# Optimization experiments

Hardware: AMD Instinct MI355X
Metric: run time of the kernel (lower is better)

Reference implementation:

```python
import jax, jax.numpy as jnp
import numpy as np

M, N = 4096, 4096

def _make_expk(n):
    k = np.arange(n, dtype=np.float64) * np.pi / (2.0 * n)
    return jnp.asarray(np.stack([np.cos(k), np.sin(k)], axis=-1), dtype=jnp.float32)

def setup_inputs() -> dict:
    key = jax.random.key(0)
    x = jax.random.normal(key, (M, N), dtype=jnp.float32)
    return {"x": x, "expkM": _make_expk(M), "expkN": _make_expk(N)}

def _idct_last(X, expk):
    """1D IDCT (inverse of unnormalized DCT-II) along last axis via Makhoul's
    N-point FFT trick. expk[k] = (cos, sin) of pi*k/(2N), i.e. e^{j pi k/(2N)}."""
    n = X.shape[-1]
    Xv = X * 0.5
    # V[k] = (Xv[k] - j*Xv[n-k]) * e^{j pi k/(2n)}, with imag part 0 at k=0
    tail = -jnp.flip(Xv, axis=-1)[..., :-1]
    Vi = jnp.concatenate([jnp.zeros_like(Xv[..., :1]), tail], axis=-1)
    W = expk[:, 0] + 1j * expk[:, 1]
    V = (Xv + 1j * Vi) * W
    v = jnp.fft.ifft(V, axis=-1).real.astype(X.dtype)
    # de-interleave: out[2m] = v[m], out[2m+1] = v[n-1-m]
    out = jnp.zeros_like(X)
    out = out.at[..., 0::2].set(v[..., : n - n // 2])
    out = out.at[..., 1::2].set(jnp.flip(v, axis=-1)[..., : n // 2])
    return out

def reference(x, expkM, expkN):
    # separable 2D IDCT: last axis (N) then first axis (M)
    y = _idct_last(x, expkN)
    y = _idct_last(y.T, expkM).T
    return y
```

## Files before the change

### kernel.cpp

```cpp
#include <hip/hip_runtime.h>
#include <math.h>


#define TT 256

constexpr float W64R[32] = {
    1.0f, 0.995184726672197f, 0.980785280403230f, 0.956940335732209f,
    0.923879532511287f, 0.881921264348355f, 0.831469612302545f, 0.773010453362737f,
    0.707106781186548f, 0.634393284163645f, 0.555570233019602f, 0.471396736825998f,
    0.382683432365090f, 0.290284677254462f, 0.195090322016128f, 0.0980171403295606f,
    0.0f, -0.0980171403295606f, -0.195090322016128f, -0.290284677254462f,
    -0.382683432365090f, -0.471396736825998f, -0.555570233019602f, -0.634393284163645f,
    -0.707106781186548f, -0.773010453362737f, -0.831469612302545f, -0.881921264348355f,
    -0.923879532511287f, -0.956940335732209f, -0.980785280403230f, -0.995184726672197f};
constexpr float W64I[32] = {
    0.0f, 0.0980171403295606f, 0.195090322016128f, 0.290284677254462f,
    0.382683432365090f, 0.471396736825998f, 0.555570233019602f, 0.634393284163645f,
    0.707106781186548f, 0.773010453362737f, 0.831469612302545f, 0.881921264348355f,
    0.923879532511287f, 0.956940335732209f, 0.980785280403230f, 0.995184726672197f,
    1.0f, 0.995184726672197f, 0.980785280403230f, 0.956940335732209f,
    0.923879532511287f, 0.881921264348355f, 0.831469612302545f, 0.773010453362737f,
    0.707106781186548f, 0.634393284163645f, 0.555570233019602f, 0.471396736825998f,
    0.382683432365090f, 0.290284677254462f, 0.195090322016128f, 0.0980171403295606f};

__device__ __forceinline__ constexpr int brev(int x, int bits) {
    int r = 0;
    for (int i = 0; i < bits; ++i) { r = (r << 1) | (x & 1); x >>= 1; }
    return r;
}

__device__ __forceinline__ float vadd(float a, float b) { return a + b; }
__device__ __forceinline__ float vsub(float a, float b) { return a - b; }
__device__ __forceinline__ float vmul(float a, float s) { return a * s; }
__device__ __forceinline__ float2 vadd(float2 a, float2 b) { return make_float2(a.x + b.x, a.y + b.y); }
__device__ __forceinline__ float2 vsub(float2 a, float2 b) { return make_float2(a.x - b.x, a.y - b.y); }
__device__ __forceinline__ float2 vmul(float2 a, float s) { return make_float2(a.x * s, a.y * s); }

template <int NP, typename V>
__device__ __forceinline__ void fft_dif(V* re, V* im) {
#pragma unroll
    for (int h = NP / 2; h >= 1; h >>= 1) {
#pragma unroll
        for (int b = 0; b < NP; b += 2 * h) {
#pragma unroll
            for (int k = 0; k < h; ++k) {
                V ur = re[b + k], ui = im[b + k];
                V vr = re[b + k + h], vi = im[b + k + h];
                V dr = vsub(ur, vr), di = vsub(ui, vi);
                re[b + k] = vadd(ur, vr);
                im[b + k] = vadd(ui, vi);
                float wr = W64R[k * (32 / h)], wi = W64I[k * (32 / h)];
                re[b + k + h] = vsub(vmul(dr, wr), vmul(di, wi));
                im[b + k + h] = vadd(vmul(dr, wi), vmul(di, wr));
            }
        }
    }
}

__global__ void tw_init_kernel(float2* __restrict__ tw2048,
                               float2* __restrict__ ca, float2* __restrict__ cb,
                               float2* __restrict__ cc, float2* __restrict__ cd) {
    int k = blockIdx.x * TT + threadIdx.x;
    const double s = 0.5 / 4096.0;
    double aw = M_PI * (double)k / 2048.0;
    double wr = cos(aw), wi = sin(aw);
    double a1 = M_PI * (double)k / 8192.0;
    double e1r = cos(a1), e1i = sin(a1);
    double a2 = M_PI * (double)(k + 2048) / 8192.0;
    double e2r = cos(a2), e2i = sin(a2);
    double Ar = s * ((1.0 - wi) * e1r - wr * e1i);
    double Ai = s * ((1.0 - wi) * e1i + wr * e1r);
    double Br = (k == 0) ? 0.0 : Ai;
    double Bi = (k == 0) ? 0.0 : -Ar;
    double Cr = s * ((1.0 + wi) * e2r + wr * e2i);
    double Ci = s * ((1.0 + wi) * e2i - wr * e2r);
    ca[k] = make_float2((float)Ar, (float)Ai);
    cb[k] = make_float2((float)Br, (float)Bi);
    cc[k] = make_float2((float)Cr, (float)Ci);
    cd[k] = make_float2((float)Ci, (float)-Cr);
    double at = M_PI * (double)k / 1024.0;
    tw2048[k] = make_float2((float)cos(at), (float)sin(at));
}

__global__ __launch_bounds__(TT, 4) void col_a_kernel(
    const float* __restrict__ x,
    const float2* __restrict__ ca, const float2* __restrict__ cb,
    const float2* __restrict__ cc, const float2* __restrict__ cd,
    const float2* __restrict__ tw2048, float2* __restrict__ T1) {
    int c = blockIdx.x * 64 + threadIdx.x;
    int k1 = blockIdx.y * 4 + threadIdx.y;
    float fr[32], fi[32];
#pragma unroll
    for (int k2 = 0; k2 < 32; ++k2) {
        int k = k1 + 64 * k2;
        float xa = x[(size_t)k * 4096 + c];
        float xb = x[(size_t)((4096 - k) & 4095) * 4096 + c];
        float xc = x[(size_t)(2048 + k) * 4096 + c];
        float xd = x[(size_t)(2048 - k) * 4096 + c];
        float2 A = ca[k], B = cb[k], C = cc[k], D = cd[k];
        fr[k2] = A.x * xa + B.x * xb + C.x * xc + D.x * xd;
        fi[k2] = A.y * xa + B.y * xb + C.y * xc + D.y * xd;
    }
    fft_dif<32, float>(fr, fi);
#pragma unroll
    for (int j = 0; j < 32; ++j) {
        int n2 = brev(j, 5);
        float2 w = tw2048[k1 * n2];
        float2 o = make_float2(fr[j] * w.x - fi[j] * w.y,
                               fr[j] * w.y + fi[j] * w.x);
        T1[(size_t)(k1 * 32 + n2) * 4096 + c] = o;
    }
}

__global__ __launch_bounds__(TT, 4) void col_b_kernel(
    const float2* __restrict__ T1, float* __restrict__ out) {
    __shared__ float2 EO[2][32][64];
    int tx = threadIdx.x;
    int ty = threadIdx.y;
    int tz = ty & 1;
    int g  = ty >> 1;
    int c = blockIdx.x * 64 + tx;
    int n2 = blockIdx.y * 2 + g;
    float fr[32], fi[32];
#pragma unroll
    for (int a = 0; a < 32; ++a) {
        int k1 = 2 * a + tz;
        float2 v = T1[(size_t)(k1 * 32 + n2) * 4096 + c];
        fr[a] = v.x; fi[a] = v.y;
    }
    fft_dif<32, float>(fr, fi);
#pragma unroll
    for (int gg = 0; gg < 2; ++gg) {
        if (g == gg) {
#pragma unroll
            for (int j = 0; j < 32; ++j) {
                int n = brev(j, 5);
                float vr = fr[j], vi = fi[j];
                if (tz) {
                    float wr = W64R[n], wi = W64I[n];
                    float t2 = vr * wr - vi * wi;
                    vi = vr * wi + vi * wr;
                    vr = t2;
                }
                EO[tz][n][tx] = make_float2(vr, vi);
            }
        }
        __syncthreads();
        if (g == gg) {
#pragma unroll
            for (int n = 0; n < 32; ++n) {
                float2 E  = EO[0][n][tx];
                float2 WO = EO[1][n][tx];
                float zr, zi;
                if (tz == 0) { zr = E.x + WO.x; zi = E.y + WO.y; }
                else         { zr = E.x - WO.x; zi = E.y - WO.y; }
                int n1 = tz * 32 + n;
                int m = 32 * n1 + n2;
                int r_re = (n1 < 32) ? 4 * m     : 8191 - 4 * m;
                int r_im = (n1 < 32) ? 4 * m + 2 : 8189 - 4 * m;
                out[(size_t)r_re * 4096 + c] = zr;
                out[(size_t)r_im * 4096 + c] = zi;
            }
        }
        __syncthreads();
    }
}

#define C_SQ2 0.70710678118654752440f
__device__ __forceinline__ void radix8(const float* ar, const float* ai,
                                       float* tr, float* ti) {
    float s04r = ar[0] + ar[4], s04i = ai[0] + ai[4];
    float d04r = ar[0] - ar[4], d04i = ai[0] - ai[4];
    float s26r = ar[2] + ar[6], s26i = ai[2] + ai[6];
    float d26r = ar[2] - ar[6], d26i = ai[2] - ai[6];
    float E0r = s04r + s26r, E0i = s04i + s26i;
    float E1r = d04r - d26i, E1i = d04i + d26r;
    float E2r = s04r - s26r, E2i = s04i - s26i;
    float E3r = d04r + d26i, E3i = d04i - d26r;
    float s15r = ar[1] + ar[5], s15i = ai[1] + ai[5];
    float d15r = ar[1] - ar[5], d15i = ai[1] - ai[5];
    float s37r = ar[3] + ar[7], s37i = ai[3] + ai[7];
    float d37r = ar[3] - ar[7], d37i = ai[3] - ai[7];
    float O0r = s15r + s37r, O0i = s15i + s37i;
    float O1r = d15r - d37i, O1i = d15i + d37r;
    float O2r = s15r - s37r, O2i = s15i - s37i;
    float O3r = d15r + d37i, O3i = d15i - d37r;
    float W1r = C_SQ2 * (O1r - O1i), W1i = C_SQ2 * (O1r + O1i);
    float W2r = -O2i, W2i = O2r;
    float W3r = -C_SQ2 * (O3r + O3i), W3i = C_SQ2 * (O3r - O3i);
    tr[0] = E0r + O0r; ti[0] = E0i + O0i;
    tr[4] = E0r - O0r; ti[4] = E0i - O0i;
    tr[1] = E1r + W1r; ti[1] = E1i + W1i;
    tr[5] = E1r - W1r; ti[5] = E1i - W1i;
    tr[2] = E2r + W2r; ti[2] = E2i + W2i;
    tr[6] = E2r - W2r; ti[6] = E2i - W2i;
    tr[3] = E3r + W3r; ti[3] = E3i + W3i;
    tr[7] = E3r - W3r; ti[7] = E3i - W3i;
}

__global__ __launch_bounds__(TT) void idct_rows_kernel(
    const float2* __restrict__ ca, const float2* __restrict__ cb,
    const float2* __restrict__ cc, const float2* __restrict__ cd,
    const float2* __restrict__ tw2048, float* __restrict__ io) {
    __shared__ float pool[8576];
    float* b0r = pool;
    float* b0i = pool + 2112;
    float* b1r = pool + 4224;
    float* b1i = pool + 6400;
    float* stg = pool + 4224;
    const int t = threadIdx.x;
    float* __restrict__ xr = io + (size_t)blockIdx.x * 4096;

#pragma unroll
    for (int u = 0; u < 4; ++u) {
        int idx = t + 256 * u;
        float4 v = ((const float4*)xr)[idx];
        *(float4*)&stg[4 * idx] = v;
    }
    __syncthreads();

    float zr[8], zi[8], tr[8], ti[8];
#pragma unroll
    for (int p = 0; p < 8; ++p) {
        int k = t + 256 * p;
        float xa = stg[k];
        float xb = stg[(4096 - k) & 4095];
        float xc = stg[2048 + k];
        float xd = stg[2048 - k];
        float2 A = ca[k], B = cb[k], C = cc[k], D = cd[k];
        zr[p] = A.x * xa + B.x * xb + C.x * xc + D.x * xd;
        zi[p] = A.y * xa + B.y * xb + C.y * xc + D.y * xd;
    }
    radix8(zr, zi, tr, ti);
    {
        int baseA = 8 * t + (t >> 2);
        b0r[baseA] = tr[0]; b0i[baseA] = ti[0];
#pragma unroll
        for (int q = 1; q < 8; ++q) {
            float2 w = tw2048[(t * q) & 2047];
            b0r[baseA + q] = w.x * tr[q] - w.y * ti[q];
            b0i[baseA + q] = w.x * ti[q] + w.y * tr[q];
        }
    }
    __syncthreads();
    {
        float ar[8], ai[8];
        int rb = t + (t >> 5);
#pragma unroll
        for (int p = 0; p < 8; ++p) { ar[p] = b0r[rb + 264 * p]; ai[p] = b0i[rb + 264 * p]; }
        radix8(ar, ai, tr, ti);
        int j = t >> 3, k = t & 7, wj = 8 * j;
        int baseB = 68 * j + k;
        b1r[baseB] = tr[0]; b1i[baseB] = ti[0];
#pragma unroll
        for (int q = 1; q < 8; ++q) {
            int off = baseB + 8 * q + (q >> 1);
            float2 w = tw2048[(wj * q) & 2047];
            b1r[off] = w.x * tr[q] - w.y * ti[q];
            b1i[off] = w.x * ti[q] + w.y * tr[q];
        }
    }
    __syncthreads();
    {
        float ar[8], ai[8];
        int rb = t + (t >> 4);
#pragma unroll
        for (int p = 0; p < 8; ++p) { ar[p] = b1r[rb + 272 * p]; ai[p] = b1i[rb + 272 * p]; }
        radix8(ar, ai, tr, ti);
        int j = t >> 6, wj = 64 * j, k = t & 63;
        int baseC = 528 * j + k + (k >> 5);
        b0r[baseC] = tr[0]; b0i[baseC] = ti[0];
#pragma unroll
        for (int q = 1; q < 8; ++q) {
            int off = baseC + 66 * q;
            float2 w = tw2048[(wj * q) & 2047];
            b0r[off] = w.x * tr[q] - w.y * ti[q];
            b0i[off] = w.x * ti[q] + w.y * tr[q];
        }
    }
    __syncthreads();
#pragma unroll
    for (int u = 0; u < 2; ++u) {
        int b = t + 256 * u;
        int rb = b + (b >> 5);
        int wb = b + (b >> 4);
        float a0r = b0r[rb], a0i = b0i[rb];
        float a1r = b0r[rb + 528], a1i = b0i[rb + 528];
        float a2r = b0r[rb + 1056], a2i = b0i[rb + 1056];
        float a3r = b0r[rb + 1584], a3i = b0i[rb + 1584];
        float s02r = a0r + a2r, s02i = a0i + a2i;
        float d02r = a0r - a2r, d02i = a0i - a2i;
        float s13r = a1r + a3r, s13i = a1i + a3i;
        float d13r = a1r - a3r, d13i = a1i - a3i;
        b1r[wb] = s02r + s13r;          b1i[wb] = s02i + s13i;
        b1r[wb + 544] = d02r - d13i;    b1i[wb + 544] = d02i + d13r;
        b1r[wb + 1088] = s02r - s13r;   b1i[wb + 1088] = s02i - s13i;
        b1r[wb + 1632] = d02r + d13i;   b1i[wb + 1632] = d02i - d13r;
    }
    __syncthreads();
#pragma unroll
    for (int i = 0; i < 4; ++i) {
        int s = t + 256 * i;
        int l2 = 2047 - s;
        int ms = s + (s >> 4);
        int ml = l2 + (l2 >> 4);
        float4 o = make_float4(b1r[ms], b1i[ml], b1i[ms], b1r[ml]);
        *(float4*)&xr[4 * s] = o;
    }
}

extern "C" void kernel_launch(void* const* d_in, const int* in_sizes, int n_in,
                              void* d_out, int out_size, void* d_ws, size_t ws_size,
                              hipStream_t stream) {
    const float* x = (const float*)d_in[0];
    float* out = (float*)d_out;

    float2* tw2048 = (float2*)d_ws;
    float2* ca = (float2*)((char*)d_ws + 1 * 16384);
    float2* cb = (float2*)((char*)d_ws + 2 * 16384);
    float2* cc = (float2*)((char*)d_ws + 3 * 16384);
    float2* cd = (float2*)((char*)d_ws + 4 * 16384);
    float2* T1 = (float2*)((char*)d_ws + (1 << 20));

    tw_init_kernel<<<8, TT, 0, stream>>>(tw2048, ca, cb, cc, cd);
    col_a_kernel<<<dim3(64, 16), dim3(64, 4), 0, stream>>>(x, ca, cb, cc, cd, tw2048, T1);
    col_b_kernel<<<dim3(64, 16), dim3(64, 4), 0, stream>>>(T1, out);
    idct_rows_kernel<<<4096, TT, 0, stream>>>(ca, cb, cc, cd, tw2048, out);
}
```

Measured before the change: 204.3 us.

## Stage col_a input loads through LDS with double-buffered async global_load_lds

Rewrites the first column-pass kernel so each block handles one k1 across 256 columns, with each wave fetching one of the four mirrored row streams through __builtin_amdgcn_global_load_lds into a double-buffered shared-memory tile. The next chunk's load overlaps the combine arithmetic on the current chunk. The aim is wider 16-byte coalesced loads and hiding global-memory latency that the old per-thread scalar strided loads exposed. In exchange it adds barriers, 32 KB of LDS per block, a different grid shape, and a dropped occupancy hint in launch_bounds.

```diff
diff --git a/kernel.cpp b/kernel.cpp
--- a/kernel.cpp
+++ b/kernel.cpp
@@ -82,37 +82,68 @@
     tw2048[k] = make_float2((float)cos(at), (float)sin(at));
 }
 
-__global__ __launch_bounds__(TT, 4) void col_a_kernel(
+typedef __attribute__((address_space(1))) const unsigned int* ga_u32;
+typedef __attribute__((address_space(3))) unsigned int* la_u32;
+
+#define COLA_STAGE(CH)                                                          \
+    do {                                                                        \
+        const int _b = (CH) & 1;                                                \
+        _Pragma("unroll") for (int v = 0; v < 4; ++v) {                         \
+            int k = k1 + 64 * ((CH) * 4 + v);                                   \
+            int row = (w == 0) ? k                                              \
+                    : (w == 1) ? ((4096 - k) & 4095)                            \
+                    : (w == 2) ? (2048 + k)                                     \
+                               : (2048 - k);                                    \
+            __builtin_amdgcn_global_load_lds(                                   \
+                (ga_u32)(const void*)(x + (size_t)row * 4096 + colb + 4 * l),   \
+                (la_u32)(void*)&stg[_b][v * 4 + w][4 * l], 16, 0, 0);           \
+        }                                                                       \
+    } while (0)
+
+__global__ __launch_bounds__(TT) void col_a_kernel(
     const float* __restrict__ x,
     const float2* __restrict__ ca, const float2* __restrict__ cb,
     const float2* __restrict__ cc, const float2* __restrict__ cd,
     const float2* __restrict__ tw2048, float2* __restrict__ T1) {
-    int c = blockIdx.x * 64 + threadIdx.x;
-    int k1 = blockIdx.y * 4 + threadIdx.y;
+    __shared__ float stg[2][16][256];
+    const int tx = threadIdx.x;
+    const int w = tx >> 6;
+    const int l = tx & 63;
+    const int k1 = blockIdx.y;
+    const int colb = blockIdx.x << 8;
     float fr[32], fi[32];
-#pragma unroll
-    for (int k2 = 0; k2 < 32; ++k2) {
-        int k = k1 + 64 * k2;
-        float xa = x[(size_t)k * 4096 + c];
-        float xb = x[(size_t)((4096 - k) & 4095) * 4096 + c];
-        float xc = x[(size_t)(2048 + k) * 4096 + c];
-        float xd = x[(size_t)(2048 - k) * 4096 + c];
-        float2 A = ca[k], B = cb[k], C = cc[k], D = cd[k];
-        fr[k2] = A.x * xa + B.x * xb + C.x * xc + D.x * xd;
-        fi[k2] = A.y * xa + B.y * xb + C.y * xc + D.y * xd;
+
+    COLA_STAGE(0);
+#pragma unroll
+    for (int ch = 0; ch < 8; ++ch) {
+        __syncthreads();
+        if (ch + 1 < 8) COLA_STAGE(ch + 1);
+        const int b = ch & 1;
+#pragma unroll
+        for (int v = 0; v < 4; ++v) {
+            int k2 = ch * 4 + v;
+            int k = k1 + 64 * k2;
+            float xa = stg[b][v * 4 + 0][tx];
+            float xb = stg[b][v * 4 + 1][tx];
+            float xc = stg[b][v * 4 + 2][tx];
+            float xd = stg[b][v * 4 + 3][tx];
+            float2 A = ca[k], B = cb[k], C = cc[k], D = cd[k];
+            fr[k2] = A.x * xa + B.x * xb + C.x * xc + D.x * xd;
+            fi[k2] = A.y * xa + B.y * xb + C.y * xc + D.y * xd;
+        }
     }
     fft_dif<32, float>(fr, fi);
 #pragma unroll
     for (int j = 0; j < 32; ++j) {
         int n2 = brev(j, 5);
-        float2 w = tw2048[k1 * n2];
-        float2 o = make_float2(fr[j] * w.x - fi[j] * w.y,
-                               fr[j] * w.y + fi[j] * w.x);
-        T1[(size_t)(k1 * 32 + n2) * 4096 + c] = o;
-    }
-}
-
-__global__ __launch_bounds__(TT, 4) void col_b_kernel(
+        float2 wv = tw2048[k1 * n2];
+        float2 o = make_float2(fr[j] * wv.x - fi[j] * wv.y,
+                               fr[j] * wv.y + fi[j] * wv.x);
+        T1[(size_t)(k1 * 32 + n2) * 4096 + colb + tx] = o;
+    }
+}
+
+__global__ __launch_bounds__(TT) void col_b_kernel(
     const float2* __restrict__ T1, float* __restrict__ out) {
     __shared__ float2 EO[2][32][64];
     int tx = threadIdx.x;
@@ -323,7 +354,7 @@
     float2* T1 = (float2*)((char*)d_ws + (1 << 20));
 
     tw_init_kernel<<<8, TT, 0, stream>>>(tw2048, ca, cb, cc, cd);
-    col_a_kernel<<<dim3(64, 16), dim3(64, 4), 0, stream>>>(x, ca, cb, cc, cd, tw2048, T1);
+    col_a_kernel<<<dim3(16, 64), TT, 0, stream>>>(x, ca, cb, cc, cd, tw2048, T1);
     col_b_kernel<<<dim3(64, 16), dim3(64, 4), 0, stream>>>(T1, out);
     idct_rows_kernel<<<4096, TT, 0, stream>>>(ca, cb, cc, cd, tw2048, out);
 }
```

After: 218.5 us. 6.9% more time.

## Replace shared-memory butterfly in column FFT stage with cross-half wavefront shuffles

Applied to the files above, without the earlier changes.

The second column-FFT kernel now places the even and odd k1 halves in the two 32-lane halves of a single wavefront. It combines them with __shfl_xor across lane 32 instead of staging through a shared-memory buffer with block-wide barriers. This removes the LDS traffic, both __syncthreads, and the serialized two-group loop, at the cost of only 32 contiguous columns per wave, which means narrower coalesced segments. Launch bounds on both column kernels are relaxed to a minimum of 1 block per CU, giving the compiler more registers but possibly lowering occupancy.

```diff
diff --git a/kernel.cpp b/kernel.cpp
--- a/kernel.cpp
+++ b/kernel.cpp
@@ -82,7 +82,7 @@
     tw2048[k] = make_float2((float)cos(at), (float)sin(at));
 }
 
-__global__ __launch_bounds__(TT, 4) void col_a_kernel(
+__global__ __launch_bounds__(TT, 1) void col_a_kernel(
     const float* __restrict__ x,
     const float2* __restrict__ ca, const float2* __restrict__ cb,
     const float2* __restrict__ cc, const float2* __restrict__ cd,
@@ -112,57 +112,40 @@
     }
 }
 
-__global__ __launch_bounds__(TT, 4) void col_b_kernel(
+__global__ __launch_bounds__(TT, 1) void col_b_kernel(
     const float2* __restrict__ T1, float* __restrict__ out) {
-    __shared__ float2 EO[2][32][64];
-    int tx = threadIdx.x;
-    int ty = threadIdx.y;
-    int tz = ty & 1;
-    int g  = ty >> 1;
-    int c = blockIdx.x * 64 + tx;
-    int n2 = blockIdx.y * 2 + g;
+    const int t = threadIdx.x;
+    const int wv = t >> 6;
+    const int l = t & 63;
+    const int par = l >> 5;
+    const int c = blockIdx.x * 32 + (l & 31);
+    const int n2 = blockIdx.y * 4 + wv;
     float fr[32], fi[32];
 #pragma unroll
     for (int a = 0; a < 32; ++a) {
-        int k1 = 2 * a + tz;
+        int k1 = 2 * a + par;
         float2 v = T1[(size_t)(k1 * 32 + n2) * 4096 + c];
         fr[a] = v.x; fi[a] = v.y;
     }
     fft_dif<32, float>(fr, fi);
-#pragma unroll
-    for (int gg = 0; gg < 2; ++gg) {
-        if (g == gg) {
-#pragma unroll
-            for (int j = 0; j < 32; ++j) {
-                int n = brev(j, 5);
-                float vr = fr[j], vi = fi[j];
-                if (tz) {
-                    float wr = W64R[n], wi = W64I[n];
-                    float t2 = vr * wr - vi * wi;
-                    vi = vr * wi + vi * wr;
-                    vr = t2;
-                }
-                EO[tz][n][tx] = make_float2(vr, vi);
-            }
-        }
-        __syncthreads();
-        if (g == gg) {
-#pragma unroll
-            for (int n = 0; n < 32; ++n) {
-                float2 E  = EO[0][n][tx];
-                float2 WO = EO[1][n][tx];
-                float zr, zi;
-                if (tz == 0) { zr = E.x + WO.x; zi = E.y + WO.y; }
-                else         { zr = E.x - WO.x; zi = E.y - WO.y; }
-                int n1 = tz * 32 + n;
-                int m = 32 * n1 + n2;
-                int r_re = (n1 < 32) ? 4 * m     : 8191 - 4 * m;
-                int r_im = (n1 < 32) ? 4 * m + 2 : 8189 - 4 * m;
-                out[(size_t)r_re * 4096 + c] = zr;
-                out[(size_t)r_im * 4096 + c] = zi;
-            }
-        }
-        __syncthreads();
+    const float sgn = par ? -1.0f : 1.0f;
+#pragma unroll
+    for (int j = 0; j < 32; ++j) {
+        int n = brev(j, 5);
+        float wr = par ? W64R[n] : 1.0f;
+        float wi = par ? W64I[n] : 0.0f;
+        float vr = fr[j] * wr - fi[j] * wi;
+        float vi = fr[j] * wi + fi[j] * wr;
+        float orr = __shfl_xor(vr, 32, 64);
+        float oii = __shfl_xor(vi, 32, 64);
+        float zr = orr + sgn * vr;
+        float zi = oii + sgn * vi;
+        int n1 = par ? (n + 32) : n;
+        int m = 32 * n1 + n2;
+        int r_re = (n1 < 32) ? 4 * m     : 8191 - 4 * m;
+        int r_im = (n1 < 32) ? 4 * m + 2 : 8189 - 4 * m;
+        out[(size_t)r_re * 4096 + c] = zr;
+        out[(size_t)r_im * 4096 + c] = zi;
     }
 }
 
@@ -324,6 +307,6 @@
 
     tw_init_kernel<<<8, TT, 0, stream>>>(tw2048, ca, cb, cc, cd);
     col_a_kernel<<<dim3(64, 16), dim3(64, 4), 0, stream>>>(x, ca, cb, cc, cd, tw2048, T1);
-    col_b_kernel<<<dim3(64, 16), dim3(64, 4), 0, stream>>>(T1, out);
+    col_b_kernel<<<dim3(128, 8), TT, 0, stream>>>(T1, out);
     idct_rows_kernel<<<4096, TT, 0, stream>>>(ca, cb, cc, cd, tw2048, out);
 }
```

New measurement: 195.2 us. 1.05x faster.
